# Performance work log

Measured on AMD Instinct MI355X. Metric: run time of the kernel, lower is better.

## Reference

```python
import jax, jax.numpy as jnp
import numpy as np

LATENT = 1024
RED = 4            # reduce_proj
GROUPS = 16
K = 3              # kernel_size
PAD = 1
REGIONS = 36
CPG = LATENT // GROUPS   # channels per group (in and out), = 64
NEG = 0.1                # LeakyReLU slope


def l2norm(x, axis=-1):
    # faithful to lavse l2norm: x / sqrt(sum(x^2)) with no eps
    return x / jnp.sqrt(jnp.sum(x * x, axis=axis, keepdims=True))


def leaky(x):
    return jnp.where(x > 0, x, NEG * x)


def setup_inputs() -> dict:
    key = jax.random.key(0)
    ks = jax.random.split(key, 7)
    Bi, Bc, T = 128, 32, 50
    img_embed = jax.random.normal(ks[0], (Bi, REGIONS, LATENT), jnp.float32)
    cap_embed = jax.random.normal(ks[1], (Bc, T, LATENT), jnp.float32)
    lens = jax.random.randint(ks[2], (Bc,), 1, T + 1)  # word counts in [1, T]
    qdim = LATENT // RED
    s1 = 1.0 / np.sqrt(LATENT)
    red_w = jax.random.uniform(ks[3], (LATENT, qdim), jnp.float32, -s1, s1)
    red_b = jax.random.uniform(ks[4], (qdim,), jnp.float32, -s1, s1)
    nw = LATENT * CPG * K  # out_channels * (in_channels // groups) * kernel_size
    s2 = 1.0 / np.sqrt(qdim)
    proj_w = jax.random.uniform(ks[5], (qdim, nw), jnp.float32, -s2, s2)
    proj_b = jax.random.uniform(ks[6], (nw,), jnp.float32, -s2, s2)
    return dict(img_embed=img_embed, cap_embed=cap_embed, lens=lens,
                red_w=red_w, red_b=red_b, proj_w=proj_w, proj_b=proj_b)


def reference(img_embed, cap_embed, lens, red_w, red_b, proj_w, proj_b):
    Bi = img_embed.shape[0]
    Bc, T, C = cap_embed.shape
    # masked mean over the first n_words of each caption -> (Bc, C)
    mask = (jnp.arange(T)[None, :] < lens[:, None]).astype(cap_embed.dtype)
    cap_repr = jnp.sum(cap_embed * mask[:, :, None], axis=1) / lens[:, None].astype(cap_embed.dtype)
    cap_act = leaky(cap_repr)                       # 'cap' gate, (Bc, C)
    # dynamic depthwise-grouped conv weights from reduced query
    q = cap_repr @ red_w + red_b                    # (Bc, qdim)
    w = (q @ proj_w + proj_b).reshape(Bc, LATENT, CPG, K)
    w = jax.nn.softmax(w, axis=-1)                  # weightnorm='softmax' over kernel dim
    w = w.reshape(Bc, GROUPS, CPG, CPG, K)          # (Bc, g, out/g, in/g, K)
    # grouped conv1d over 36 regions, padding=1
    img = img_embed.transpose(0, 2, 1)              # (Bi, C, L)
    imgp = jnp.pad(img, ((0, 0), (0, 0), (PAD, PAD)))
    shif = jnp.stack([imgp[:, :, k:k + REGIONS] for k in range(K)], axis=-1)  # (Bi, C, L, K)
    shif = shif.reshape(Bi, GROUPS, CPG, REGIONS, K)
    out = jnp.einsum('bgilk,ngoik->nbgol', shif, w).reshape(Bc, Bi, LATENT, REGIONS)
    out = leaky(out)
    # (x * cap).mean(-1) == x.mean(-1) * cap since cap broadcasts over positions
    img_vec = l2norm(jnp.mean(out, axis=-1) * cap_act[:, None, :])  # (Bc, Bi, C)
    cap_vec = l2norm(cap_repr)                                      # (Bc, C)
    sims = jnp.einsum('nbc,nc->bn', img_vec, cap_vec)               # (Bi, Bc)
    return sims
```

## Files before the change

### kernel.cpp

```cpp
#include <hip/hip_runtime.h>
#include <math.h>

#define LATENT 1024
#define QDIM 256
#define NW 196608
#define BI 128
#define BC 32
#define TT 50
#define REGIONS 36
#define NGROUPS 16
#define CPG 64
#define NEG 0.1f

typedef __attribute__((ext_vector_type(8))) short short8;
typedef __attribute__((ext_vector_type(16))) float f32x16;

__device__ __forceinline__ float leakyf(float x){ return x > 0.f ? x : NEG * x; }

__device__ __forceinline__ unsigned short f2bf(float x){
    union { float f; unsigned int u; } v; v.f = x;
    unsigned int r = v.u + 0x7FFFu + ((v.u >> 16) & 1u);
    return (unsigned short)(r >> 16);
}

__global__ __launch_bounds__(256) void cap_mean_kernel(
    const float* __restrict__ cap_embed, const int* __restrict__ lens,
    float* __restrict__ cap_repr, float* __restrict__ cap_act,
    float* __restrict__ norm_capr)
{
    const int n = blockIdx.x;
    const int len = lens[n];
    const float invl = 1.f / (float)len;
    const int c4 = threadIdx.x;
    const float* base = cap_embed + (size_t)n * TT * LATENT + c4 * 4;
    float4 s = {0.f, 0.f, 0.f, 0.f};
    for (int t = 0; t < len; ++t) {
        const float4 v = *reinterpret_cast<const float4*>(base + (size_t)t * LATENT);
        s.x += v.x; s.y += v.y; s.z += v.z; s.w += v.w;
    }
    float4 m = {s.x * invl, s.y * invl, s.z * invl, s.w * invl};
    *reinterpret_cast<float4*>(cap_repr + n * LATENT + c4 * 4) = m;
    const float sc = 1.f / 36.f;
    float4 a = {leakyf(m.x) * sc, leakyf(m.y) * sc, leakyf(m.z) * sc, leakyf(m.w) * sc};
    *reinterpret_cast<float4*>(cap_act + n * LATENT + c4 * 4) = a;
    float ss = m.x*m.x + m.y*m.y + m.z*m.z + m.w*m.w;
    #pragma unroll
    for (int off = 32; off; off >>= 1) ss += __shfl_xor(ss, off);
    __shared__ float red4[4];
    if ((threadIdx.x & 63) == 0) red4[threadIdx.x >> 6] = ss;
    __syncthreads();
    if (threadIdx.x == 0) norm_capr[n] = sqrtf(red4[0] + red4[1] + red4[2] + red4[3]);
}

__global__ __launch_bounds__(256) void q_kernel(
    const float* __restrict__ cap_repr, const float* __restrict__ red_w,
    const float* __restrict__ red_b, unsigned short* __restrict__ qbfF)
{
    const int cg = blockIdx.x, n = blockIdx.y;
    const int col = threadIdx.x & 31, ks = threadIdx.x >> 5;
    const float* cr = cap_repr + n * LATENT;
    float p = 0.f;
    const int r0 = ks * 128;
    for (int r = r0; r < r0 + 128; ++r)
        p = fmaf(cr[r], red_w[(size_t)r * QDIM + cg * 32 + col], p);
    __shared__ float part[256];
    part[threadIdx.x] = p;
    __syncthreads();
    if (threadIdx.x < 32) {
        float s = red_b[cg * 32 + col];
        #pragma unroll
        for (int k = 0; k < 8; ++k) s += part[k * 32 + col];
        const int r = cg * 32 + col;
        const int elem = (r >> 4) * 512 + ((r >> 3) & 1) * 256 + n * 8 + (r & 7);
        qbfF[elem] = f2bf(s);
    }
}

__global__ __launch_bounds__(384) void wgen8_kernel(
    const unsigned short* __restrict__ qbfF, const float* __restrict__ proj_w,
    const float* __restrict__ proj_b, unsigned short* __restrict__ Wp2F)
{
    __shared__ unsigned short Bst[2][3072];
    __shared__ float L[192 * 33];
    const int tid = threadIdx.x;
    const int g = blockIdx.x >> 6, o = blockIdx.x & 63;
    const int colbase = (g * 64 + o) * 192;
    const int wv = tid >> 6, lane = tid & 63;
    const int lrow = lane & 31, khalf = lane >> 5;

    short8 afr[16];
    {
        const unsigned short* qp = qbfF + (size_t)lane * 8;
        #pragma unroll
        for (int s = 0; s < 16; ++s)
            afr[s] = *reinterpret_cast<const short8*>(qp + s * 512);
    }

    const int c4 = tid % 48;
    const int rp = tid / 48;
    const int c0 = c4 * 4;
    const int kh_w = rp >> 2;
    const int j0 = (rp * 2) & 7;

    float4 A0, A1;
    {
        const float* src = proj_w + (size_t)(rp * 2) * NW + colbase + c0;
        A0 = *reinterpret_cast<const float4*>(src);
        A1 = *reinterpret_cast<const float4*>(src + NW);
    }

    f32x16 acc = {};
    for (int s = 0; s < 16; ++s) {
        __syncthreads();
        unsigned short* Bb = Bst[s & 1];
        {
            const float a0[4] = {A0.x, A0.y, A0.z, A0.w};
            const float a1[4] = {A1.x, A1.y, A1.z, A1.w};
            #pragma unroll
            for (int cc = 0; cc < 4; ++cc) {
                const int col = c0 + cc;
                const unsigned int lo = f2bf(a0[cc]);
                const unsigned int hi = f2bf(a1[cc]);
                const int ei = (col >> 5) * 512 + kh_w * 256 + (col & 31) * 8 + j0;
                *reinterpret_cast<unsigned int*>(&Bb[ei]) = lo | (hi << 16);
            }
        }
        if (s < 15) {
            const float* src = proj_w + (size_t)((s + 1) * 16 + rp * 2) * NW + colbase + c0;
            A0 = *reinterpret_cast<const float4*>(src);
            A1 = *reinterpret_cast<const float4*>(src + NW);
        }
        __syncthreads();
        const short8 bf = *reinterpret_cast<const short8*>(&Bb[wv * 512 + lane * 8]);
        acc = __builtin_amdgcn_mfma_f32_32x32x16_bf16(afr[s], bf, acc, 0, 0, 0);
    }

    const int col_local = wv * 32 + lrow;
    const float pb = proj_b[colbase + col_local];
    #pragma unroll
    for (int reg = 0; reg < 16; ++reg) {
        const int n = (reg & 3) + 8 * (reg >> 2) + 4 * khalf;
        L[col_local * 33 + n] = acc[reg] + pb;
    }
    __syncthreads();

    const int nt = o >> 5, lrow_o = o & 63 & 31;
    for (int idx = tid; idx < 2048; idx += 384) {
        const int n = idx & 31, i = idx >> 5;
        const int c = i * 3;
        const float x0 = L[c * 33 + n], x1 = L[(c+1)*33 + n], x2 = L[(c+2)*33 + n];
        const float m = fmaxf(fmaxf(x0, x1), x2);
        const float e0 = expf(x0 - m), e1 = expf(x1 - m), e2 = expf(x2 - m);
        const float inv = 1.f / (e0 + e1 + e2);
        const int ks = i >> 4, kh = (i >> 3) & 1, j = i & 7;
        const size_t base = (size_t)(n * 16 + g) * 12288
                          + (size_t)(nt * 4 + ks) * 512
                          + kh * 256 + lrow_o * 8 + j;
        Wp2F[base]        = f2bf(e0 * inv);
        Wp2F[base + 4096] = f2bf(e1 * inv);
        Wp2F[base + 8192] = f2bf(e2 * inv);
    }
}

__global__ __launch_bounds__(576, 3) void conv5_kernel(
    const float* __restrict__ img_embed, const unsigned short* __restrict__ Wp2F,
    const float* __restrict__ cap_repr, const float* __restrict__ cap_act,
    float* __restrict__ part_dot, float* __restrict__ part_ss)
{
    const int g = blockIdx.x, bt = blockIdx.y, nq = blockIdx.z;
    const int b0 = bt * 8;
    __shared__ int4 BsmV[3072];
    char* BsmRaw = (char*)BsmV;
    __shared__ float Sw[2][9][2][64];
    const int tid = threadIdx.x;
    const int wv = tid >> 6, lane = tid & 63;
    const int lrow = lane & 31, khalf = lane >> 5;
    const int ioff = khalf * 16;

    const float* imgG = img_embed + (size_t)b0 * 36 * 1024 + g * 64;
    for (int idx = tid; idx < 2304; idx += 576) {
        const int row_img = idx >> 3, ch = idx & 7;
        const int bbs = row_img / 36;
        const int l = row_img - bbs * 36;
        const float* src = imgG + (size_t)row_img * 1024 + ch * 8;
        const float4 u = *reinterpret_cast<const float4*>(src);
        const float4 v = *reinterpret_cast<const float4*>(src + 4);
        unsigned short r8[8];
        r8[0]=f2bf(u.x); r8[1]=f2bf(u.y); r8[2]=f2bf(u.z); r8[3]=f2bf(u.w);
        r8[4]=f2bf(v.x); r8[5]=f2bf(v.y); r8[6]=f2bf(v.z); r8[7]=f2bf(v.w);
        const int arow = bbs * 38 + l + 1;
        const int byte = (arow * 128 + ch * 16) ^ ((arow & 7) << 4);
        *reinterpret_cast<int4*>(BsmRaw + byte) = *reinterpret_cast<const int4*>(r8);
    }
    if (tid < 128) {
        const int rr = tid >> 3, ch = tid & 7;
        const int arow = (rr >> 1) * 38 + (rr & 1) * 37;
        const int byte = (arow * 128 + ch * 16) ^ ((arow & 7) << 4);
        int4 z; z.x = 0; z.y = 0; z.z = 0; z.w = 0;
        *reinterpret_cast<int4*>(BsmRaw + byte) = z;
    }
    __syncthreads();

    const int rg = wv * 32 + lrow;
    const int bbr = rg / 36;
    const int abase = bbr * 38 + (rg - bbr * 36);
    short8 afr[3][4];
    #pragma unroll
    for (int k = 0; k < 3; ++k)
        #pragma unroll
        for (int ks = 0; ks < 4; ++ks) {
            const int arow = abase + k;
            const int byte = (arow * 128 + ks * 32 + ioff) ^ ((arow & 7) << 4);
            afr[k][ks] = *reinterpret_cast<const short8*>(BsmRaw + byte);
        }
    const int rbase = wv * 32;
    const int bfirst = rbase / 36;
    const int bsplit = (bfirst + 1) * 36 - rbase;
    __syncthreads();

    const int n0 = nq * 16;
    int4 st0, st1, st2;
    {
        const unsigned short* WF = Wp2F + (size_t)(n0 * 16 + g) * 12288;
        st0 = *reinterpret_cast<const int4*>(WF + (size_t)tid * 8);
        st1 = *reinterpret_cast<const int4*>(WF + (size_t)(tid + 576) * 8);
        if (tid < 384) st2 = *reinterpret_cast<const int4*>(WF + (size_t)(tid + 1152) * 8);
        *reinterpret_cast<int4*>(BsmRaw + (size_t)tid * 16) = st0;
        *reinterpret_cast<int4*>(BsmRaw + (size_t)(tid + 576) * 16) = st1;
        if (tid < 384) *reinterpret_cast<int4*>(BsmRaw + (size_t)(tid + 1152) * 16) = st2;
    }
    __syncthreads();

    for (int ni = 0; ni < 16; ++ni) {
        const int n = n0 + ni;
        char* Bcur = BsmRaw + (size_t)(ni & 1) * 24576;
        char* Bnxt = BsmRaw + (size_t)((ni + 1) & 1) * 24576;

        if (ni < 15) {
            const unsigned short* WF = Wp2F + (size_t)((n + 1) * 16 + g) * 12288;
            st0 = *reinterpret_cast<const int4*>(WF + (size_t)tid * 8);
            st1 = *reinterpret_cast<const int4*>(WF + (size_t)(tid + 576) * 8);
            if (tid < 384) st2 = *reinterpret_cast<const int4*>(WF + (size_t)(tid + 1152) * 8);
        }

        f32x16 acc0 = {}, acc1 = {};
        #pragma unroll
        for (int k = 0; k < 3; ++k) {
            #pragma unroll
            for (int ks = 0; ks < 4; ++ks) {
                const char* fb = Bcur + k * 8192 + ks * 1024 + (size_t)lane * 16;
                const short8 bf0 = *reinterpret_cast<const short8*>(fb);
                const short8 bf1 = *reinterpret_cast<const short8*>(fb + 4096);
                acc0 = __builtin_amdgcn_mfma_f32_32x32x16_bf16(afr[k][ks], bf0, acc0, 0, 0, 0);
                acc1 = __builtin_amdgcn_mfma_f32_32x32x16_bf16(afr[k][ks], bf1, acc1, 0, 0, 0);
            }
        }

        if (ni < 15) {
            *reinterpret_cast<int4*>(Bnxt + (size_t)tid * 16) = st0;
            *reinterpret_cast<int4*>(Bnxt + (size_t)(tid + 576) * 16) = st1;
            if (tid < 384) *reinterpret_cast<int4*>(Bnxt + (size_t)(tid + 1152) * 16) = st2;
        }

        float s0A = 0.f, s0B = 0.f, s1A = 0.f, s1B = 0.f;
        #pragma unroll
        for (int reg = 0; reg < 16; ++reg) {
            const int rit = (reg & 3) + 8 * (reg >> 2) + 4 * khalf;
            const float v0 = leakyf(acc0[reg]);
            const float v1 = leakyf(acc1[reg]);
            if (rit >= bsplit) { s0B += v0; s1B += v1; }
            else               { s0A += v0; s1A += v1; }
        }
        s0A += __shfl_xor(s0A, 32); s0B += __shfl_xor(s0B, 32);
        s1A += __shfl_xor(s1A, 32); s1B += __shfl_xor(s1B, 32);
        const int q = ni & 1;
        if (khalf == 0) {
            Sw[q][wv][0][lrow]      = s0A;
            Sw[q][wv][0][32 + lrow] = s1A;
            if (bsplit < 32) {
                Sw[q][wv][1][lrow]      = s0B;
                Sw[q][wv][1][32 + lrow] = s1B;
            }
        }
        __syncthreads();

        if (tid < 128) {
            const int b = tid >> 4, j = tid & 15;
            const float4 ca4 = *reinterpret_cast<const float4*>(&cap_act [n * LATENT + g * CPG + j * 4]);
            const float4 cr4 = *reinterpret_cast<const float4*>(&cap_repr[n * LATENT + g * CPG + j * 4]);
            const float cav[4] = {ca4.x, ca4.y, ca4.z, ca4.w};
            const float crv[4] = {cr4.x, cr4.y, cr4.z, cr4.w};
            float d = 0.f, ss = 0.f;
            #pragma unroll
            for (int u = 0; u < 4; ++u) {
                const int o = j * 4 + u;
                const float S = (b == 0)
                    ? Sw[q][0][0][o] + Sw[q][1][0][o]
                    : Sw[q][b][1][o] + Sw[q][b + 1][0][o];
                const float tmp = S * cav[u];
                d = fmaf(tmp, crv[u], d);
                ss = fmaf(tmp, tmp, ss);
            }
            #pragma unroll
            for (int off = 1; off <= 8; off <<= 1) {
                d += __shfl_xor(d, off);
                ss += __shfl_xor(ss, off);
            }
            if (j == 0) {
                part_dot[((size_t)n * BI + b0 + b) * NGROUPS + g] = d;
                part_ss [((size_t)n * BI + b0 + b) * NGROUPS + g] = ss;
            }
        }
    }
}

__global__ __launch_bounds__(256) void final_kernel(
    const float* __restrict__ part_dot, const float* __restrict__ part_ss,
    const float* __restrict__ norm_capr, float* __restrict__ out)
{
    const int idx = blockIdx.x * 256 + threadIdx.x;
    const int n = idx & 31;
    const int b = idx >> 5;
    const size_t base = ((size_t)n * BI + b) * NGROUPS;
    float d = 0.f, s = 0.f;
    #pragma unroll
    for (int g = 0; g < NGROUPS; ++g) { d += part_dot[base + g]; s += part_ss[base + g]; }
    out[b * BC + n] = d / (sqrtf(s) * norm_capr[n]);
}

extern "C" void kernel_launch(void* const* d_in, const int* in_sizes, int n_in,
                              void* d_out, int out_size, void* d_ws, size_t ws_size,
                              hipStream_t stream) {
    const float* img_embed = (const float*)d_in[0];
    const float* cap_embed = (const float*)d_in[1];
    const int*   lens      = (const int*)  d_in[2];
    const float* red_w     = (const float*)d_in[3];
    const float* red_b     = (const float*)d_in[4];
    const float* proj_w    = (const float*)d_in[5];
    const float* proj_b    = (const float*)d_in[6];
    float* out = (float*)d_out;

    char* ws = (char*)d_ws;
    unsigned short* Wp2F   = (unsigned short*)(ws);
    float* cap_repr  = (float*)(ws + 22020096);
    float* cap_act   = (float*)(ws + 22151168);
    unsigned short* qbfF = (unsigned short*)(ws + 22282240);
    float* norm_capr = (float*)(ws + 22315008);
    float* part_dot  = (float*)(ws + 22315520);
    float* part_ss   = (float*)(ws + 22577664);

    hipLaunchKernelGGL(cap_mean_kernel, dim3(BC), dim3(256), 0, stream,
                       cap_embed, lens, cap_repr, cap_act, norm_capr);
    hipLaunchKernelGGL(q_kernel, dim3(8, BC), dim3(256), 0, stream,
                       cap_repr, red_w, red_b, qbfF);
    hipLaunchKernelGGL(wgen8_kernel, dim3(1024), dim3(384), 0, stream,
                       qbfF, proj_w, proj_b, Wp2F);
    hipLaunchKernelGGL(conv5_kernel, dim3(NGROUPS, 16, 2), dim3(576), 0, stream,
                       img_embed, Wp2F, cap_repr, cap_act, part_dot, part_ss);
    hipLaunchKernelGGL(final_kernel, dim3(16), dim3(256), 0, stream,
                       part_dot, part_ss, norm_capr, out);
}
```

Baseline: 186.5 us.

## Load proj_w directly into MFMA A-fragments, removing LDS staging in weight generation

The weight-generation kernel now has each lane load its own proj_w column values straight into registers and swaps the MFMA operand roles, so proj_w is the A operand and the query fragments are B. This removes the shared-memory double buffer and the two barriers per k-step. The cost is uncoalesced-looking scalar loads: each lane reads 8 strided rows, with 32 consecutive columns per half-wave. The bias is staged in LDS and the accumulator scatter is transposed to match the new layout.

```diff
diff --git a/kernel.cpp b/kernel.cpp
--- a/kernel.cpp
+++ b/kernel.cpp
@@ -76,75 +76,61 @@
     }
 }
 
-__global__ __launch_bounds__(384) void wgen8_kernel(
+__global__ __launch_bounds__(384) void wgen9_kernel(
     const unsigned short* __restrict__ qbfF, const float* __restrict__ proj_w,
     const float* __restrict__ proj_b, unsigned short* __restrict__ Wp2F)
 {
-    __shared__ unsigned short Bst[2][3072];
     __shared__ float L[192 * 33];
+    __shared__ float pbs[192];
     const int tid = threadIdx.x;
     const int g = blockIdx.x >> 6, o = blockIdx.x & 63;
     const int colbase = (g * 64 + o) * 192;
     const int wv = tid >> 6, lane = tid & 63;
     const int lrow = lane & 31, khalf = lane >> 5;
 
-    short8 afr[16];
+    if (tid < 192) pbs[tid] = proj_b[colbase + tid];
+
+    short8 qfr[16];
     {
         const unsigned short* qp = qbfF + (size_t)lane * 8;
         #pragma unroll
         for (int s = 0; s < 16; ++s)
-            afr[s] = *reinterpret_cast<const short8*>(qp + s * 512);
-    }
-
-    const int c4 = tid % 48;
-    const int rp = tid / 48;
-    const int c0 = c4 * 4;
-    const int kh_w = rp >> 2;
-    const int j0 = (rp * 2) & 7;
-
-    float4 A0, A1;
-    {
-        const float* src = proj_w + (size_t)(rp * 2) * NW + colbase + c0;
-        A0 = *reinterpret_cast<const float4*>(src);
-        A1 = *reinterpret_cast<const float4*>(src + NW);
-    }
+            qfr[s] = *reinterpret_cast<const short8*>(qp + s * 512);
+    }
+
+    const float* pw0 = proj_w + (size_t)(khalf * 8) * NW + colbase + wv * 32 + lrow;
+
+    float a[8], b[8];
+    #pragma unroll
+    for (int j = 0; j < 8; ++j) a[j] = pw0[(size_t)j * NW];
 
     f32x16 acc = {};
+    #pragma unroll
     for (int s = 0; s < 16; ++s) {
-        __syncthreads();
-        unsigned short* Bb = Bst[s & 1];
-        {
-            const float a0[4] = {A0.x, A0.y, A0.z, A0.w};
-            const float a1[4] = {A1.x, A1.y, A1.z, A1.w};
+        if (s < 15) {
+            const float* pwn = pw0 + (size_t)((s + 1) * 16) * NW;
             #pragma unroll
-            for (int cc = 0; cc < 4; ++cc) {
-                const int col = c0 + cc;
-                const unsigned int lo = f2bf(a0[cc]);
-                const unsigned int hi = f2bf(a1[cc]);
-                const int ei = (col >> 5) * 512 + kh_w * 256 + (col & 31) * 8 + j0;
-                *reinterpret_cast<unsigned int*>(&Bb[ei]) = lo | (hi << 16);
-            }
-        }
-        if (s < 15) {
-            const float* src = proj_w + (size_t)((s + 1) * 16 + rp * 2) * NW + colbase + c0;
-            A0 = *reinterpret_cast<const float4*>(src);
-            A1 = *reinterpret_cast<const float4*>(src + NW);
-        }
-        __syncthreads();
-        const short8 bf = *reinterpret_cast<const short8*>(&Bb[wv * 512 + lane * 8]);
-        acc = __builtin_amdgcn_mfma_f32_32x32x16_bf16(afr[s], bf, acc, 0, 0, 0);
-    }
-
-    const int col_local = wv * 32 + lrow;
-    const float pb = proj_b[colbase + col_local];
+            for (int j = 0; j < 8; ++j) b[j] = pwn[(size_t)j * NW];
+        }
+        unsigned short u[8];
+        #pragma unroll
+        for (int j = 0; j < 8; ++j) u[j] = f2bf(a[j]);
+        const short8 af = *reinterpret_cast<const short8*>(u);
+        acc = __builtin_amdgcn_mfma_f32_32x32x16_bf16(af, qfr[s], acc, 0, 0, 0);
+        #pragma unroll
+        for (int j = 0; j < 8; ++j) a[j] = b[j];
+    }
+
+    __syncthreads();
     #pragma unroll
     for (int reg = 0; reg < 16; ++reg) {
-        const int n = (reg & 3) + 8 * (reg >> 2) + 4 * khalf;
-        L[col_local * 33 + n] = acc[reg] + pb;
-    }
-    __syncthreads();
-
-    const int nt = o >> 5, lrow_o = o & 63 & 31;
+        const int rit = (reg & 3) + 8 * (reg >> 2) + 4 * khalf;
+        const int c = wv * 32 + rit;
+        L[c * 33 + lrow] = acc[reg] + pbs[c];
+    }
+    __syncthreads();
+
+    const int nt = o >> 5, lrow_o = o & 31;
     for (int idx = tid; idx < 2048; idx += 384) {
         const int n = idx & 31, i = idx >> 5;
         const int c = i * 3;
@@ -353,7 +339,7 @@
                        cap_embed, lens, cap_repr, cap_act, norm_capr);
     hipLaunchKernelGGL(q_kernel, dim3(8, BC), dim3(256), 0, stream,
                        cap_repr, red_w, red_b, qbfF);
-    hipLaunchKernelGGL(wgen8_kernel, dim3(1024), dim3(384), 0, stream,
+    hipLaunchKernelGGL(wgen9_kernel, dim3(1024), dim3(384), 0, stream,
                        qbfF, proj_w, proj_b, Wp2F);
     hipLaunchKernelGGL(conv5_kernel, dim3(NGROUPS, 16, 2), dim3(576), 0, stream,
                        img_embed, Wp2F, cap_repr, cap_act, part_dot, part_ss);
```

Measured after the change: 180.8 us. -3.0%, faster.
